# Kernel optimization log

Hardware: AMD Instinct MI355X
Metric: run time of the kernel (lower is better)

Reference implementation:

```python
import jax, jax.numpy as jnp
import numpy as np

H_DIM = 1024
N_HEADS = 16
HEAD_DIM = H_DIM // N_HEADS
MAX_POS = 2048   # RotaryEmbedding default max_position_embeddings
BASE = 10000.0
SCALING_FACTOR = 1.0


def rotate_half(x):
    # interleaved convention: cat([-x[..., 1::2], x[..., ::2]], -1)
    return jnp.concatenate([-x[..., 1::2], x[..., ::2]], axis=-1)


def rope_cos_sin(seq_len, dtype):
    # LlamaDynamicNTKScalingRotaryEmbedding._set_cos_sin_cache
    base = BASE
    if seq_len > MAX_POS:
        base = BASE * (SCALING_FACTOR * seq_len / MAX_POS - (SCALING_FACTOR - 1.0)) ** (HEAD_DIM / (HEAD_DIM - 2))
    inv_freq = 1.0 / (base ** (jnp.arange(0, HEAD_DIM, 2, dtype=jnp.float32) / HEAD_DIM))
    t = jnp.arange(seq_len, dtype=jnp.float32)
    freqs = jnp.einsum('i,j->ij', t, inv_freq)          # [S, D/2]
    emb = jnp.concatenate([freqs, freqs], axis=-1)       # [S, D]
    return emb.astype(dtype), jnp.cos(emb).astype(dtype), jnp.sin(emb).astype(dtype)


def setup_inputs() -> dict:
    key = jax.random.key(0)
    ks = jax.random.split(key, 5)
    B, S = 1, 4096
    scale_w = 0.02
    return {
        'hidden_states': jax.random.normal(ks[0], (B, S, H_DIM), dtype=jnp.float32),
        'Wq': jax.random.normal(ks[1], (H_DIM, H_DIM), dtype=jnp.float32) * scale_w,
        'Wk': jax.random.normal(ks[2], (H_DIM, H_DIM), dtype=jnp.float32) * scale_w,
        'Wv': jax.random.normal(ks[3], (H_DIM, H_DIM), dtype=jnp.float32) * scale_w,
        'Wo': jax.random.normal(ks[4], (H_DIM, H_DIM), dtype=jnp.float32) * scale_w,
    }


def reference(hidden_states, Wq, Wk, Wv, Wo):
    B, S, H = hidden_states.shape
    # projections (nn.Linear: x @ W.T)
    def proj(x, W):
        y = jnp.einsum('bsh,oh->bso', x, W)
        return y.reshape(B, S, N_HEADS, HEAD_DIM).transpose(0, 2, 1, 3)  # bhsd
    q = proj(hidden_states, Wq)
    k = proj(hidden_states, Wk)
    v = proj(hidden_states, Wv)

    _, cos, sin = rope_cos_sin(S, hidden_states.dtype)
    cos = cos[None, None, :, :]   # [1,1,S,D] (position_ids = arange(S)[None], unsqueeze(1))
    sin = sin[None, None, :, :]
    q = q * cos + rotate_half(q) * sin
    k = k * cos + rotate_half(k) * sin

    # NOTE: source DIVIDES by scale = head_dim**-0.5 (i.e. multiplies by sqrt(d))
    scale = HEAD_DIM ** (-0.5)
    attn = jnp.einsum('bhsd,bhtd->bhst', q, k) / scale
    attn = jax.nn.softmax(attn, axis=-1)
    out = jnp.einsum('bhst,bhtd->bhsd', attn, v)
    out = out.transpose(0, 2, 1, 3).reshape(B, S, H)
    return jnp.einsum('bsh,oh->bso', out, Wo)
```

## Files before the change

### kernel.cpp

```cpp
#include <hip/hip_runtime.h>
#include <cmath>
#include <cstdint>

#define S_LEN 4096
#define NH 16
#define HD 64

typedef _Float16 f16x8 __attribute__((ext_vector_type(8)));
typedef __attribute__((ext_vector_type(4))) float f32x4;
typedef __attribute__((ext_vector_type(16))) float f32x16;
typedef __attribute__((ext_vector_type(4))) unsigned short u16x4;
typedef __attribute__((ext_vector_type(4))) unsigned int u32x4;
typedef __attribute__((ext_vector_type(4))) float f4;

__device__ __forceinline__ unsigned short f2h(float x) {
  union { _Float16 h; unsigned short u; } v; v.h = (_Float16)x; return v.u;
}
__device__ __forceinline__ float permx32(float v) {
  int idx = (((int)(threadIdx.x & 63)) ^ 32) << 2;
  return __int_as_float(__builtin_amdgcn_ds_bpermute(idx, __float_as_int(v)));
}
__device__ __forceinline__ unsigned permx32u(unsigned v) {
  int idx = (((int)(threadIdx.x & 63)) ^ 32) << 2;
  return (unsigned)__builtin_amdgcn_ds_bpermute(idx, (int)v);
}
__device__ __forceinline__ float exp2a(float x) {
  float r; asm("v_exp_f32 %0, %1" : "=v"(r) : "v"(x)); return r;
}
__device__ __forceinline__ unsigned pkh(float a, float b) {
  unsigned r;
  asm("v_cvt_pkrtz_f16_f32 %0, %1, %2" : "=v"(r) : "v"(a), "v"(b));
  return r;
}

#define GLL16(g, l) __builtin_amdgcn_global_load_lds( \
    (const __attribute__((address_space(1))) void*)(g), \
    (__attribute__((address_space(3))) void*)(l), 16, 0, 0)

#define PLANE_BYTES 524288
#define TILE_BYTES 8192

__global__ __launch_bounds__(256) void cvt_kernel(
    const float* __restrict__ hs, const float* __restrict__ wq,
    const float* __restrict__ wk, const float* __restrict__ wv,
    const float* __restrict__ wo,
    unsigned short* __restrict__ hs16,
    unsigned short* __restrict__ wq16, unsigned short* __restrict__ wk16,
    unsigned short* __restrict__ wv16, unsigned short* __restrict__ wo16)
{
  const int HID4 = (S_LEN * 1024) / 4;
  const int W4   = (1024 * 1024) / 4;
  const int total = HID4 + 4 * W4;
  for (int i = blockIdx.x * 256 + threadIdx.x; i < total;
       i += gridDim.x * 256) {
    const float* s; unsigned short* d; int off;
    if (i < HID4) { s = hs; d = hs16; off = i; }
    else {
      int j = i - HID4; int w = j >> 18; off = j & (W4 - 1);
      s = (w == 0) ? wq : (w == 1) ? wk : (w == 2) ? wv : wo;
      d = (w == 0) ? wq16 : (w == 1) ? wk16 : (w == 2) ? wv16 : wo16;
    }
    f4 v = *(const f4*)(s + (size_t)off * 4);
    u16x4 r;
#pragma unroll
    for (int j = 0; j < 4; j++) r[j] = f2h(v[j]);
    *(u16x4*)(d + (size_t)off * 4) = r;
  }
}

__global__ __launch_bounds__(256) void rope_table(
    float* __restrict__ cosT, float* __restrict__ sinT, double base)
{
  int idx = blockIdx.x * 256 + threadIdx.x;
  if (idx >= S_LEN * 32) return;
  int t = idx >> 5, j = idx & 31;
  double invf = pow(base, -(double)j / 32.0);
  double f = fmod((double)t * invf, 6.283185307179586476925286766559);
  float ff = (float)f;
  cosT[idx] = cosf(ff);
  sinT[idx] = sinf(ff);
}

__global__ __launch_bounds__(256) void gemm_f16(
    const unsigned short* __restrict__ A,
    const unsigned short* __restrict__ B0, const unsigned short* __restrict__ B1,
    const unsigned short* __restrict__ B2,
    void* O0, void* O1, void* O2, int M, int K, int fin)
{
  __shared__ unsigned short As[128 * 64];
  __shared__ unsigned short Bs[128 * 64];
  const int z = blockIdx.z;
  const unsigned short* B = (z == 0) ? B0 : (z == 1) ? B1 : B2;
  void* O = (z == 0) ? O0 : (z == 1) ? O1 : O2;
  const int m0 = blockIdx.y * 128, n0 = blockIdx.x * 128;
  const int tid = threadIdx.x, wid = tid >> 6, lane = tid & 63;
  const int lr = lane & 15, lk = (lane >> 4) * 8;
  const int wr = (wid >> 1) * 64, wc = (wid & 1) * 64;
  const int strow = lane >> 3;
  const int stcol = (lane & 7) * 8;

  f32x4 acc[4][4];
#pragma unroll
  for (int m = 0; m < 4; m++)
#pragma unroll
    for (int n = 0; n < 4; n++) acc[m][n] = (f32x4){0.f, 0.f, 0.f, 0.f};

  for (int kt = 0; kt < K; kt += 64) {
#pragma unroll
    for (int i = 0; i < 4; i++) {
      int c = wid * 4 + i;
      int row = c * 8 + strow;
      GLL16(A + (size_t)(m0 + row) * K + kt + stcol, &As[c * 512]);
      GLL16(B + (size_t)(n0 + row) * K + kt + stcol, &Bs[c * 512]);
    }
    __syncthreads();
    f16x8 af[4][2], bfr[4][2];
#pragma unroll
    for (int m = 0; m < 4; m++)
#pragma unroll
      for (int kk = 0; kk < 2; kk++)
        af[m][kk] = *(const f16x8*)&As[(wr + m * 16 + lr) * 64 + kk * 32 + lk];
#pragma unroll
    for (int n = 0; n < 4; n++)
#pragma unroll
      for (int kk = 0; kk < 2; kk++)
        bfr[n][kk] = *(const f16x8*)&Bs[(wc + n * 16 + lr) * 64 + kk * 32 + lk];
#pragma unroll
    for (int m = 0; m < 4; m++)
#pragma unroll
      for (int n = 0; n < 4; n++)
#pragma unroll
        for (int kk = 0; kk < 2; kk++)
          acc[m][n] = __builtin_amdgcn_mfma_f32_16x16x32_f16(
              af[m][kk], bfr[n][kk], acc[m][n], 0, 0, 0);
    __syncthreads();
  }

  const int rbase = m0 + wr + (lane >> 4) * 4;
  const int cbase = n0 + wc + lr;
  if (fin) {
    float* C = (float*)O;
#pragma unroll
    for (int m = 0; m < 4; m++)
#pragma unroll
      for (int n = 0; n < 4; n++)
#pragma unroll
        for (int j = 0; j < 4; j++) {
          int s = rbase + m * 16 + j;
          int o = cbase + n * 16;
          C[(size_t)s * 1024 + o] = acc[m][n][j];
        }
  } else if (z == 2) {
    char* base = (char*)O;
#pragma unroll
    for (int m = 0; m < 4; m++)
#pragma unroll
      for (int n = 0; n < 4; n++) {
        int s = rbase + m * 16;
        int o = cbase + n * 16;
        int hd = o >> 6, d = o & 63;
        size_t tb = (size_t)hd * PLANE_BYTES + (size_t)(s >> 6) * TILE_BYTES
                  + (size_t)d * 128;
        int cbyte = (2 * (s & 63)) ^ ((d & 7) << 4);
        u16x4 r;
#pragma unroll
        for (int j = 0; j < 4; j++) r[j] = f2h(acc[m][n][j]);
        *(u16x4*)(base + tb + cbyte) = r;
      }
  } else {
    float* C = (float*)O;
#pragma unroll
    for (int m = 0; m < 4; m++)
#pragma unroll
      for (int n = 0; n < 4; n++)
#pragma unroll
        for (int j = 0; j < 4; j++) {
          int s = rbase + m * 16 + j;
          int o = cbase + n * 16;
          C[((size_t)(o >> 6) * M + s) * HD + (o & 63)] = acc[m][n][j];
        }
  }
}

__global__ __launch_bounds__(256) void rope_apply(
    const float* __restrict__ Qf, const float* __restrict__ Kf,
    unsigned short* __restrict__ Q16, char* __restrict__ Kt,
    const float* __restrict__ cosT, const float* __restrict__ sinT)
{
  int wid = threadIdx.x >> 6, lane = threadIdx.x & 63;
  int row = blockIdx.x * 4 + wid;
  int t = row & (S_LEN - 1);
  int head = row >> 12;
  int j = (lane < 32) ? lane : (lane - 32);
  float c = cosT[t * 32 + j], s = sinT[t * 32 + j];
  int partner = (lane < 32) ? (2 * lane + 1) : (2 * (lane - 32));
  float sgn = (lane < 32) ? -1.0f : 1.0f;
  const float* qp = Qf + (size_t)row * HD;
  const float* kp = Kf + (size_t)row * HD;
  float q = qp[lane], k = kp[lane];
  float qo = __shfl(q, partner, 64);
  float ko = __shfl(k, partner, 64);
  float qr = (q * c + sgn * qo * s) * 11.541560327111707f;
  float kr = k * c + sgn * ko * s;
  Q16[(size_t)row * HD + lane] = f2h(qr);
  size_t kb = (size_t)head * PLANE_BYTES + (size_t)(t >> 6) * TILE_BYTES
            + (size_t)(t & 63) * 128 + ((2 * lane) ^ ((t & 7) << 4));
  *(unsigned short*)(Kt + kb) = f2h(kr);
}

__global__ __launch_bounds__(256, 2) void attn_kernel(
    const unsigned short* __restrict__ Q16, const char* __restrict__ Kt,
    const char* __restrict__ Vt, unsigned short* __restrict__ Oattn)
{
  __shared__ char KL[2][TILE_BYTES];
  __shared__ char VL[2][TILE_BYTES];

  const int tid = threadIdx.x, wid = tid >> 6, lane = tid & 63;
  const int l5 = lane & 31, hi2 = lane >> 5;
  const bool lohalf = (hi2 == 0);

  int id = blockIdx.x + 32 * blockIdx.y;
  int h  = (id & 7) + 8 * ((id >> 3) & 1);
  int bx = id >> 4;
  const int qw = bx * 128 + wid * 32;

  const size_t hoff = (size_t)h * PLANE_BYTES;
  const char* KtH = Kt + hoff;
  const char* VtH = Vt + hoff;

  const unsigned short* Qrow = Q16 + ((size_t)h * S_LEN + qw + l5) * HD;
  f16x8 qf[4];
#pragma unroll
  for (int ks = 0; ks < 4; ks++)
    qf[ks] = *(const f16x8*)&Qrow[ks * 16 + hi2 * 8];

  f32x16 o0 = (f32x16)0.0f, o1 = (f32x16)0.0f;
  float m_q = -__builtin_inff(), l_q = 0.f;

#define STAGE(kt, b) do { \
    size_t tb = (size_t)(kt) * TILE_BYTES; \
    _Pragma("unroll") \
    for (int c = 0; c < 2; c++) { \
      int ub = c * 4096 + wid * 1024; \
      int go = ub + lane * 16; \
      GLL16(KtH + tb + go, &KL[b][ub]); \
      GLL16(VtH + tb + go, &VL[b][ub]); \
    } } while (0)

  STAGE(0, 0);

  const int NT = S_LEN / 64;
  for (int kt = 0; kt < NT; ++kt) {
    const int cur = kt & 1;
    asm volatile("s_waitcnt vmcnt(0)" ::: "memory");
    __builtin_amdgcn_s_barrier();
    asm volatile("" ::: "memory");

    if (kt + 1 < NT) STAGE(kt + 1, cur ^ 1);

    f32x16 s0 = (f32x16)0.0f, s1 = (f32x16)0.0f;
    __builtin_amdgcn_s_setprio(1);
#pragma unroll
    for (int ks = 0; ks < 4; ks++) {
      const int coff = (32 * ks + 16 * hi2) ^ ((l5 & 7) << 4);
      f16x8 k0 = *(const f16x8*)(&KL[cur][l5 * 128 + coff]);
      f16x8 k1 = *(const f16x8*)(&KL[cur][(32 + l5) * 128 + coff]);
      s0 = __builtin_amdgcn_mfma_f32_32x32x16_f16(k0, qf[ks], s0, 0, 0, 0);
      s1 = __builtin_amdgcn_mfma_f32_32x32x16_f16(k1, qf[ks], s1, 0, 0, 0);
    }
    __builtin_amdgcn_s_setprio(0);

    float mx = fmaxf(s0[0], s1[0]);
#pragma unroll
    for (int r = 1; r < 16; r++) mx = fmaxf(mx, fmaxf(s0[r], s1[r]));
    mx = fmaxf(mx, permx32(mx));

    if (__any(mx > m_q + 11.0f)) {
      float mnew = fmaxf(m_q, mx);
      float alpha = exp2a(m_q - mnew);
      m_q = mnew;
      l_q *= alpha;
#pragma unroll
      for (int i = 0; i < 16; i++) { o0[i] *= alpha; o1[i] *= alpha; }
    }

    f16x8 pf[4];
    float rs = 0.f;
#pragma unroll
    for (int ks = 0; ks < 4; ks++) {
      f32x16 sv = (ks < 2) ? s0 : s1;
      const int base = (ks & 1) * 8;
      float e0 = exp2a(sv[base + 0] - m_q);
      float e1 = exp2a(sv[base + 1] - m_q);
      float e2 = exp2a(sv[base + 2] - m_q);
      float e3 = exp2a(sv[base + 3] - m_q);
      float e4 = exp2a(sv[base + 4] - m_q);
      float e5 = exp2a(sv[base + 5] - m_q);
      float e6 = exp2a(sv[base + 6] - m_q);
      float e7 = exp2a(sv[base + 7] - m_q);
      rs += ((e0 + e1) + (e2 + e3)) + ((e4 + e5) + (e6 + e7));
      unsigned a0 = pkh(e0, e1);
      unsigned a1 = pkh(e2, e3);
      unsigned b0 = pkh(e4, e5);
      unsigned b1 = pkh(e6, e7);
      unsigned sw0 = permx32u(lohalf ? b0 : a0);
      unsigned sw1 = permx32u(lohalf ? b1 : a1);
      u32x4 w;
      w[0] = lohalf ? a0 : sw0;
      w[1] = lohalf ? a1 : sw1;
      w[2] = lohalf ? sw0 : b0;
      w[3] = lohalf ? sw1 : b1;
      union { u32x4 u; f16x8 f; } cv; cv.u = w;
      pf[ks] = cv.f;
    }
    rs += permx32(rs);
    l_q += rs;

    __builtin_amdgcn_s_setprio(1);
#pragma unroll
    for (int ks = 0; ks < 4; ks++) {
      const int coff = (32 * ks + 16 * hi2) ^ ((l5 & 7) << 4);
      f16x8 v0 = *(const f16x8*)(&VL[cur][l5 * 128 + coff]);
      f16x8 v1 = *(const f16x8*)(&VL[cur][(32 + l5) * 128 + coff]);
      o0 = __builtin_amdgcn_mfma_f32_32x32x16_f16(v0, pf[ks], o0, 0, 0, 0);
      o1 = __builtin_amdgcn_mfma_f32_32x32x16_f16(v1, pf[ks], o1, 0, 0, 0);
    }
    __builtin_amdgcn_s_setprio(0);
  }
#undef STAGE

  const float inv = 1.0f / l_q;
  unsigned* orow = (unsigned*)(Oattn + (size_t)(qw + l5) * 1024 + h * HD);
#pragma unroll
  for (int k = 0; k < 8; k++) {
    const int d0 = 2 * (k & 1) + 8 * (k >> 1) + 4 * hi2;
    orow[d0 >> 1]        = pkh(o0[2 * k] * inv, o0[2 * k + 1] * inv);
    orow[(d0 + 32) >> 1] = pkh(o1[2 * k] * inv, o1[2 * k + 1] * inv);
  }
}

extern "C" void kernel_launch(void* const* d_in, const int* in_sizes, int n_in,
                              void* d_out, int out_size, void* d_ws, size_t ws_size,
                              hipStream_t stream)
{
  const float* hs = (const float*)d_in[0];
  const float* Wq = (const float*)d_in[1];
  const float* Wk = (const float*)d_in[2];
  const float* Wv = (const float*)d_in[3];
  const float* Wo = (const float*)d_in[4];

  char* ws = (char*)d_ws;
  const size_t HS = (size_t)S_LEN * 1024;
  const size_t WN = (size_t)1024 * 1024;
  size_t off = 0;
  unsigned short* hs16 = (unsigned short*)(ws + off); off += HS * 2;
  unsigned short* wq16 = (unsigned short*)(ws + off); off += WN * 2;
  unsigned short* wk16 = (unsigned short*)(ws + off); off += WN * 2;
  unsigned short* wv16 = (unsigned short*)(ws + off); off += WN * 2;
  unsigned short* wo16 = (unsigned short*)(ws + off); off += WN * 2;
  float* Qf = (float*)(ws + off); off += HS * 4;
  float* Kf = (float*)(ws + off); off += HS * 4;
  char* VT_g = ws + off; off += (size_t)NH * PLANE_BYTES;
  char* Kt_g = ws + off; off += (size_t)NH * PLANE_BYTES;
  float* cosT = (float*)(ws + off); off += (size_t)S_LEN * 32 * 4;
  float* sinT = (float*)(ws + off); off += (size_t)S_LEN * 32 * 4;
  unsigned short* Q16 = hs16;
  unsigned short* Ab  = (unsigned short*)Qf;

  cvt_kernel<<<4096, 256, 0, stream>>>(hs, Wq, Wk, Wv, Wo,
                                       hs16, wq16, wk16, wv16, wo16);

  double base = 10000.0 * pow((double)S_LEN / 2048.0, 64.0 / 62.0);
  rope_table<<<(S_LEN * 32 + 255) / 256, 256, 0, stream>>>(cosT, sinT, base);

  gemm_f16<<<dim3(8, 32, 3), 256, 0, stream>>>(
      hs16, wq16, wk16, wv16, Qf, Kf, VT_g, S_LEN, 1024, 0);

  rope_apply<<<NH * S_LEN / 4, 256, 0, stream>>>(
      Qf, Kf, Q16, Kt_g, cosT, sinT);

  attn_kernel<<<dim3(32, 16), 256, 0, stream>>>(
      Q16, Kt_g, VT_g, Ab);

  gemm_f16<<<dim3(8, 32, 1), 256, 0, stream>>>(
      Ab, wo16, wo16, wo16, d_out, d_out, d_out, S_LEN, 1024, 1);
}
```

Measured before the change: 213.2 us.

## Split attention KV range in two with combine kernel; store Q/K projections as fp16

```diff
diff --git a/kernel.cpp b/kernel.cpp
--- a/kernel.cpp
+++ b/kernel.cpp
@@ -15,6 +15,9 @@
 
 __device__ __forceinline__ unsigned short f2h(float x) {
   union { _Float16 h; unsigned short u; } v; v.h = (_Float16)x; return v.u;
+}
+__device__ __forceinline__ float h2f(unsigned short u) {
+  union { unsigned short u; _Float16 h; } v; v.u = u; return (float)v.h;
 }
 __device__ __forceinline__ float permx32(float v) {
   int idx = (((int)(threadIdx.x & 63)) ^ 32) << 2;
@@ -168,7 +171,7 @@
         *(u16x4*)(base + tb + cbyte) = r;
       }
   } else {
-    float* C = (float*)O;
+    unsigned short* C = (unsigned short*)O;
 #pragma unroll
     for (int m = 0; m < 4; m++)
 #pragma unroll
@@ -177,13 +180,13 @@
         for (int j = 0; j < 4; j++) {
           int s = rbase + m * 16 + j;
           int o = cbase + n * 16;
-          C[((size_t)(o >> 6) * M + s) * HD + (o & 63)] = acc[m][n][j];
+          C[((size_t)(o >> 6) * M + s) * HD + (o & 63)] = f2h(acc[m][n][j]);
         }
   }
 }
 
 __global__ __launch_bounds__(256) void rope_apply(
-    const float* __restrict__ Qf, const float* __restrict__ Kf,
+    const unsigned short* __restrict__ Qh, const unsigned short* __restrict__ Kh,
     unsigned short* __restrict__ Q16, char* __restrict__ Kt,
     const float* __restrict__ cosT, const float* __restrict__ sinT)
 {
@@ -195,9 +198,8 @@
   float c = cosT[t * 32 + j], s = sinT[t * 32 + j];
   int partner = (lane < 32) ? (2 * lane + 1) : (2 * (lane - 32));
   float sgn = (lane < 32) ? -1.0f : 1.0f;
-  const float* qp = Qf + (size_t)row * HD;
-  const float* kp = Kf + (size_t)row * HD;
-  float q = qp[lane], k = kp[lane];
+  float q = h2f(Qh[(size_t)row * HD + lane]);
+  float k = h2f(Kh[(size_t)row * HD + lane]);
   float qo = __shfl(q, partner, 64);
   float ko = __shfl(k, partner, 64);
   float qr = (q * c + sgn * qo * s) * 11.541560327111707f;
@@ -208,9 +210,10 @@
   *(unsigned short*)(Kt + kb) = f2h(kr);
 }
 
-__global__ __launch_bounds__(256, 2) void attn_kernel(
+__global__ __launch_bounds__(256, 4) void attn_kernel(
     const unsigned short* __restrict__ Q16, const char* __restrict__ Kt,
-    const char* __restrict__ Vt, unsigned short* __restrict__ Oattn)
+    const char* __restrict__ Vt,
+    unsigned short* __restrict__ Opart, float* __restrict__ Ml)
 {
   __shared__ char KL[2][TILE_BYTES];
   __shared__ char VL[2][TILE_BYTES];
@@ -218,6 +221,7 @@
   const int tid = threadIdx.x, wid = tid >> 6, lane = tid & 63;
   const int l5 = lane & 31, hi2 = lane >> 5;
   const bool lohalf = (hi2 == 0);
+  const int z = blockIdx.z;
 
   int id = blockIdx.x + 32 * blockIdx.y;
   int h  = (id & 7) + 8 * ((id >> 3) & 1);
@@ -237,8 +241,11 @@
   f32x16 o0 = (f32x16)0.0f, o1 = (f32x16)0.0f;
   float m_q = -__builtin_inff(), l_q = 0.f;
 
+  const int T0 = z * 32;
+  const int NT = 32;
+
 #define STAGE(kt, b) do { \
-    size_t tb = (size_t)(kt) * TILE_BYTES; \
+    size_t tb = (size_t)(T0 + (kt)) * TILE_BYTES; \
     _Pragma("unroll") \
     for (int c = 0; c < 2; c++) { \
       int ub = c * 4096 + wid * 1024; \
@@ -249,7 +256,6 @@
 
   STAGE(0, 0);
 
-  const int NT = S_LEN / 64;
   for (int kt = 0; kt < NT; ++kt) {
     const int cur = kt & 1;
     asm volatile("s_waitcnt vmcnt(0)" ::: "memory");
@@ -330,12 +336,48 @@
 #undef STAGE
 
   const float inv = 1.0f / l_q;
-  unsigned* orow = (unsigned*)(Oattn + (size_t)(qw + l5) * 1024 + h * HD);
+  const int q = qw + l5;
+  unsigned* orow = (unsigned*)(Opart + (((size_t)(z * NH + h)) * S_LEN + q) * HD);
 #pragma unroll
   for (int k = 0; k < 8; k++) {
     const int d0 = 2 * (k & 1) + 8 * (k >> 1) + 4 * hi2;
     orow[d0 >> 1]        = pkh(o0[2 * k] * inv, o0[2 * k + 1] * inv);
     orow[(d0 + 32) >> 1] = pkh(o1[2 * k] * inv, o1[2 * k + 1] * inv);
+  }
+  if (hi2 == 0) {
+    float2* mlp = (float2*)Ml + ((size_t)(z * NH + h)) * S_LEN + q;
+    *mlp = make_float2(m_q, l_q);
+  }
+}
+
+__global__ __launch_bounds__(256) void combine_kernel(
+    const unsigned short* __restrict__ Opart, const float* __restrict__ Ml,
+    unsigned short* __restrict__ Ab)
+{
+  const int NQ = S_LEN * 1024 / 4;
+  for (int idx = blockIdx.x * 256 + threadIdx.x; idx < NQ;
+       idx += gridDim.x * 256) {
+    int e = idx * 4;
+    int s = e >> 10;
+    int col = e & 1023;
+    int h = col >> 6, d = col & 63;
+    const float2* mlb = (const float2*)Ml;
+    float2 ml0 = mlb[(size_t)h * S_LEN + s];
+    float2 ml1 = mlb[(size_t)(NH + h) * S_LEN + s];
+    float mmax = fmaxf(ml0.x, ml1.x);
+    float w0 = exp2f(ml0.x - mmax) * ml0.y;
+    float w1 = exp2f(ml1.x - mmax) * ml1.y;
+    float rden = 1.0f / (w0 + w1);
+    float c0 = w0 * rden, c1 = w1 * rden;
+    const unsigned short* p0 = Opart + ((size_t)h * S_LEN + s) * HD + d;
+    const unsigned short* p1 = Opart + ((size_t)(NH + h) * S_LEN + s) * HD + d;
+    u16x4 a = *(const u16x4*)p0;
+    u16x4 b = *(const u16x4*)p1;
+    u16x4 r;
+#pragma unroll
+    for (int j = 0; j < 4; j++)
+      r[j] = f2h(c0 * h2f(a[j]) + c1 * h2f(b[j]));
+    *(u16x4*)(Ab + e) = r;
   }
 }
 
@@ -358,14 +400,16 @@
   unsigned short* wk16 = (unsigned short*)(ws + off); off += WN * 2;
   unsigned short* wv16 = (unsigned short*)(ws + off); off += WN * 2;
   unsigned short* wo16 = (unsigned short*)(ws + off); off += WN * 2;
-  float* Qf = (float*)(ws + off); off += HS * 4;
-  float* Kf = (float*)(ws + off); off += HS * 4;
+  unsigned short* Qh16 = (unsigned short*)(ws + off); off += HS * 2;
+  unsigned short* Kh16 = (unsigned short*)(ws + off); off += HS * 2;
+  char* Kt_g = ws + off; off += (size_t)NH * PLANE_BYTES;
   char* VT_g = ws + off; off += (size_t)NH * PLANE_BYTES;
-  char* Kt_g = ws + off; off += (size_t)NH * PLANE_BYTES;
+  unsigned short* Ab = (unsigned short*)(ws + off); off += HS * 2;
+  float* Ml = (float*)(ws + off); off += (size_t)2 * NH * S_LEN * 8;
   float* cosT = (float*)(ws + off); off += (size_t)S_LEN * 32 * 4;
   float* sinT = (float*)(ws + off); off += (size_t)S_LEN * 32 * 4;
   unsigned short* Q16 = hs16;
-  unsigned short* Ab  = (unsigned short*)Qf;
+  unsigned short* Opart = Qh16;
 
   cvt_kernel<<<4096, 256, 0, stream>>>(hs, Wq, Wk, Wv, Wo,
                                        hs16, wq16, wk16, wv16, wo16);
@@ -374,13 +418,15 @@
   rope_table<<<(S_LEN * 32 + 255) / 256, 256, 0, stream>>>(cosT, sinT, base);
 
   gemm_f16<<<dim3(8, 32, 3), 256, 0, stream>>>(
-      hs16, wq16, wk16, wv16, Qf, Kf, VT_g, S_LEN, 1024, 0);
+      hs16, wq16, wk16, wv16, Qh16, Kh16, VT_g, S_LEN, 1024, 0);
 
   rope_apply<<<NH * S_LEN / 4, 256, 0, stream>>>(
-      Qf, Kf, Q16, Kt_g, cosT, sinT);
-
-  attn_kernel<<<dim3(32, 16), 256, 0, stream>>>(
-      Q16, Kt_g, VT_g, Ab);
+      Qh16, Kh16, Q16, Kt_g, cosT, sinT);
+
+  attn_kernel<<<dim3(32, 16, 2), 256, 0, stream>>>(
+      Q16, Kt_g, VT_g, Opart, Ml);
+
+  combine_kernel<<<2048, 256, 0, stream>>>(Opart, Ml, Ab);
 
   gemm_f16<<<dim3(8, 32, 1), 256, 0, stream>>>(
       Ab, wo16, wo16, wo16, d_out, d_out, d_out, S_LEN, 1024, 1);
```

Result: no change. 209.4 us (-1.8%).
